# Optimization experiments

Measured on AMD Instinct MI355X. Metric: run time of the kernel, lower is better.

Reference implementation:

```python
import jax, jax.numpy as jnp
import numpy as np

M, K, N, R = 8192, 4096, 4096, 64  # tokens, in_features, out_features, pod_rank


def _unpack_int4(packed):
    """Unpack bytes (stored as int32 in [0,256)) into signed int4 values in [-8,7].
    Low nibble is element 2k, high nibble is element 2k+1."""
    b = packed.astype(jnp.int32)
    low = ((b & 0xF) ^ 8) - 8
    high = (((b >> 4) & 0xF) ^ 8) - 8
    out = jnp.stack([low, high], axis=-1)
    return out.reshape(packed.shape[:-1] + (packed.shape[-1] * 2,))


def setup_inputs() -> dict:
    key = jax.random.key(0)
    ks = jax.random.split(key, 7)
    x_quant = jax.random.randint(ks[0], (M, K // 2), 0, 256, dtype=jnp.int32)
    x_scale = jax.random.uniform(ks[1], (M,), dtype=jnp.float32) * 0.01 + 1e-4
    weight = jax.random.randint(ks[2], (N, K // 2), 0, 256, dtype=jnp.int32)
    weight_scales = jax.random.uniform(ks[3], (N, 1), dtype=jnp.float32) * 0.01 + 1e-4
    bias = jax.random.normal(ks[4], (N,), dtype=jnp.float32) * 0.02
    x_r = jax.random.normal(ks[5], (M, R), dtype=jnp.float32)
    w_outlier = jax.random.normal(ks[6], (N, R), dtype=jnp.float32) * 0.02
    return {"x_quant": x_quant, "x_scale": x_scale, "weight": weight,
            "weight_scales": weight_scales, "bias": bias, "x_r": x_r,
            "w_outlier": w_outlier}


def reference(x_quant, x_scale, weight, weight_scales, bias, x_r, w_outlier):
    xi = _unpack_int4(x_quant)          # [M, K] int32 in [-8,7]
    wi = _unpack_int4(weight)           # [N, K] int32 in [-8,7]
    y_int = jnp.matmul(xi, wi.T)        # [M, N] int32 accumulator
    # dequant: per-token activation scale * per-channel weight scale, plus bias
    y = (y_int.astype(jnp.float32) * x_scale[:, None] * weight_scales.reshape(1, -1)
         + bias[None, :])
    # fused low-rank outlier correction: addmm_(x_r, w_outlier.T)
    y = y + jnp.matmul(x_r, w_outlier.T)
    return y
```

## Files before the change

### kernel.cpp

```cpp
#include <hip/hip_runtime.h>
#include <hip/hip_fp16.h>

typedef int      v4i  __attribute__((ext_vector_type(4)));
typedef int      v2i  __attribute__((ext_vector_type(2)));
typedef int      v16i __attribute__((ext_vector_type(16)));
typedef float    v4f  __attribute__((ext_vector_type(4)));
typedef float    v16f __attribute__((ext_vector_type(16)));
typedef _Float16 v8h  __attribute__((ext_vector_type(8)));
typedef _Float16 v4h  __attribute__((ext_vector_type(4)));

#define MDIM 8192
#define NDIM 4096
#define KDIM 4096
#define RDIM 64
#define KW   (KDIM / 2)
#define NT   (KDIM / 128)

typedef const __attribute__((address_space(1))) char* gas_ptr;
typedef __attribute__((address_space(3))) char*       las_ptr;

__device__ __forceinline__ void unpack_w(v4i w, int& lo8, int& hi8) {
    unsigned p01 = __builtin_amdgcn_perm((unsigned)w.y, (unsigned)w.x, 0x0C0C0400u);
    unsigned p23 = __builtin_amdgcn_perm((unsigned)w.w, (unsigned)w.z, 0x0C0C0400u);
    unsigned b4  = __builtin_amdgcn_perm(p23, p01, 0x05040100u);
    unsigned lo = b4 & 0x0F0F0F0Fu;
    unsigned hi = (b4 >> 4) & 0x0F0F0F0Fu;
    lo8 = (int)(((lo ^ 0x08080808u) + 0x78787878u) ^ 0x80808080u);
    hi8 = (int)(((hi ^ 0x08080808u) + 0x78787878u) ^ 0x80808080u);
}

__global__ __launch_bounds__(256)
void repack_int4(const int* __restrict__ xq, const int* __restrict__ wq,
                 char* __restrict__ x8, char* __restrict__ w8)
{
    const size_t XCH = (size_t)MDIM * KW / 4;
    const size_t TCH = XCH + (size_t)NDIM * KW / 4;
    size_t stride = (size_t)gridDim.x * blockDim.x;
    for (size_t i = (size_t)blockIdx.x * blockDim.x + threadIdx.x; i < TCH; i += stride) {
        const int* src;
        char* dst;
        if (i < XCH) { src = xq + i * 4; dst = x8 + i * 8; }
        else { size_t j = i - XCH; src = wq + j * 4; dst = w8 + j * 8; }
        v4i w = *(const v4i*)src;
        int lo8, hi8;
        unpack_w(w, lo8, hi8);
        *(v2i*)dst = (v2i){lo8, hi8};
    }
}

__device__ __forceinline__ void stage2(const char* g, char* l, int kt, int ks) {
    const char* s = g + kt * 128 + ks * 64;
    __builtin_amdgcn_global_load_lds((gas_ptr)(const void*)s,
                                     (las_ptr)(void*)l, 16, 0, 0);
    __builtin_amdgcn_global_load_lds((gas_ptr)(const void*)(s + (size_t)128 * KDIM),
                                     (las_ptr)(void*)(l + 8192), 16, 0, 0);
}

#define BAR asm volatile("s_barrier" ::: "memory")
#define VM4 asm volatile("s_waitcnt vmcnt(4)" ::: "memory")
#define SGB(m, n) __builtin_amdgcn_sched_group_barrier(m, n, 0)

#define SGBSEQ do {                                                            \
    SGB(0x100, 2); SGB(0x8, 2); SGB(0x100, 2); SGB(0x8, 2);                    \
    SGB(0x100, 2); SGB(0x8, 2); SGB(0x100, 2); SGB(0x8, 2);                    \
    SGB(0x100, 2); SGB(0x8, 2); SGB(0x100, 2); SGB(0x8, 2);                    \
    SGB(0x30, 2);  SGB(0x8, 2); SGB(0x30, 2);  SGB(0x8, 2);                    \
} while (0)

#define READ_AB(DA, DB, PAR, KS_) do {                                         \
    const char* Ab_ = (const char*)Asub[PAR][KS_];                             \
    const char* Bb_ = (const char*)Bsub[PAR][KS_];                             \
    _Pragma("unroll")                                                          \
    for (int ii = 0; ii < 4; ++ii) {                                           \
        DA[ii][0] = *(const v4i*)(Ab_ + aoff + ii * 2048);                     \
        DA[ii][1] = *(const v4i*)(Ab_ + (aoff ^ 32) + ii * 2048);              \
    }                                                                          \
    _Pragma("unroll")                                                          \
    for (int jj = 0; jj < 2; ++jj) {                                           \
        DB[jj][0] = *(const v4i*)(Bb_ + boff + jj * 2048);                     \
        DB[jj][1] = *(const v4i*)(Bb_ + (boff ^ 32) + jj * 2048);              \
    }                                                                          \
} while (0)

#define MMA16(AS, BS)                                                          \
    _Pragma("unroll")                                                          \
    for (int ks_ = 0; ks_ < 2; ++ks_)                                          \
        _Pragma("unroll")                                                      \
        for (int ii = 0; ii < 4; ++ii)                                         \
            _Pragma("unroll")                                                  \
            for (int jj = 0; jj < 2; ++jj)                                     \
                acc[ii][jj] = __builtin_amdgcn_mfma_i32_32x32x32_i8(           \
                    AS[ii][ks_], BS[jj][ks_], acc[ii][jj], 0, 0, 0)

#define QPHASE(CA, CB, NA, NB, NPAR, NKS, SPAR, SKS, SKT) do {                 \
    READ_AB(NA, NB, NPAR, NKS);                                                \
    stage2(gA, &Asub[SPAR][SKS][ldsW], SKT, SKS);                              \
    stage2(gB, &Bsub[SPAR][SKS][ldsW], SKT, SKS);                              \
    MMA16(CA, CB);                                                             \
    SGBSEQ;                                                                    \
    VM4; BAR;                                                                  \
} while (0)

__global__ __launch_bounds__(512, 2)
void w4a4_g32(const char* __restrict__ x8, const char* __restrict__ w8,
              const float* __restrict__ xsc, const float* __restrict__ wsc,
              const float* __restrict__ bias, const float* __restrict__ xr,
              const float* __restrict__ wo, float* __restrict__ out)
{
    __shared__ __align__(16) char Asub[2][2][16384];
    __shared__ __align__(16) char Bsub[2][2][16384];
    __shared__ float xs_s[256];
    __shared__ float ws_s[256];
    __shared__ float bs_s[256];

    const int tid  = threadIdx.x;
    const int lane = tid & 63;
    const int wid  = tid >> 6;
    const int wm   = wid >> 2;
    const int wn   = wid & 3;

    const int s  = (blockIdx.x & 7) * 64 + (blockIdx.x >> 3);
    const int by = s >> 4;
    const int bxn = s & 15;

    if (tid < 256) {
        xs_s[tid] = xsc[by * 256 + tid];
    } else {
        int n = tid - 256;
        ws_s[n] = wsc[bxn * 256 + n];
        bs_s[n] = bias[bxn * 256 + n];
    }

    const int srow = wid * 16 + (lane >> 2);
    const int scol = ((lane & 3) * 16) ^ (((lane >> 3) & 3) << 4);
    const char* gA = x8 + (size_t)(by * 256 + srow) * KDIM + scol;
    const char* gB = w8 + (size_t)(bxn * 256 + srow) * KDIM + scol;
    const int ldsW = wid * 1024;

    const int l31 = lane & 31;
    const int kh  = lane >> 5;
    const int cks = (kh << 4) ^ (((l31 >> 1) & 3) << 4);
    const int aoff = (wm * 128 + l31) * 64 + cks;
    const int boff = (wn * 64  + l31) * 64 + cks;

    v16i acc[4][2];
#pragma unroll
    for (int i = 0; i < 4; ++i)
#pragma unroll
        for (int j = 0; j < 2; ++j)
#pragma unroll
            for (int r = 0; r < 16; ++r) acc[i][j][r] = 0;

    stage2(gA, &Asub[0][0][ldsW], 0, 0);
    stage2(gB, &Bsub[0][0][ldsW], 0, 0);
    stage2(gA, &Asub[0][1][ldsW], 0, 1);
    stage2(gB, &Bsub[0][1][ldsW], 0, 1);
    stage2(gA, &Asub[1][0][ldsW], 1, 0);
    stage2(gB, &Bsub[1][0][ldsW], 1, 0);
    VM4;
    BAR;

    v4i a0[4][2], b0[2][2], a1[4][2], b1[2][2];
    READ_AB(a0, b0, 0, 0);

    for (int it = 0; it < NT / 2; ++it) {
        const int kt1 = 2 * it + 1;
        const int kt2 = (2 * it + 2 < NT) ? 2 * it + 2 : NT - 1;
        const int kt3 = (2 * it + 3 < NT) ? 2 * it + 3 : NT - 1;
        QPHASE(a0, b0, a1, b1, 0, 1, 1, 1, kt1);
        QPHASE(a1, b1, a0, b0, 1, 0, 0, 0, kt2);
        QPHASE(a0, b0, a1, b1, 1, 1, 0, 1, kt2);
        QPHASE(a1, b1, a0, b0, 0, 0, 1, 0, kt3);
    }

    asm volatile("s_waitcnt vmcnt(0)" ::: "memory");
    BAR;

    char* Xh = (char*)&Asub[0][0][0];
    char* Wh = (char*)&Bsub[0][0][0];
    {
        const int rr = tid >> 3;
        const int cb = (tid & 7) * 16;
#pragma unroll
        for (int p = 0; p < 4; ++p) {
            const int row = p * 64 + rr;
            const int sw = cb ^ ((row & 7) << 4);
            v4f x0 = *(const v4f*)(xr + (size_t)(by * 256 + row) * RDIM + (cb >> 1));
            v4f x1 = *(const v4f*)(xr + (size_t)(by * 256 + row) * RDIM + (cb >> 1) + 4);
            v8h hx = {(_Float16)x0[0], (_Float16)x0[1], (_Float16)x0[2], (_Float16)x0[3],
                      (_Float16)x1[0], (_Float16)x1[1], (_Float16)x1[2], (_Float16)x1[3]};
            *(v8h*)(Xh + (size_t)row * 128 + sw) = hx;
            v4f w0 = *(const v4f*)(wo + (size_t)(bxn * 256 + row) * RDIM + (cb >> 1));
            v4f w1 = *(const v4f*)(wo + (size_t)(bxn * 256 + row) * RDIM + (cb >> 1) + 4);
            v8h hw = {(_Float16)w0[0], (_Float16)w0[1], (_Float16)w0[2], (_Float16)w0[3],
                      (_Float16)w1[0], (_Float16)w1[1], (_Float16)w1[2], (_Float16)w1[3]};
            *(v8h*)(Wh + (size_t)row * 128 + sw) = hw;
        }
    }

#pragma unroll
    for (int i = 0; i < 4; ++i) {
        const int r0 = wm * 128 + i * 32 + kh * 4;
#pragma unroll
        for (int j = 0; j < 2; ++j) {
            const int col = wn * 64 + j * 32 + l31;
            const float sw = ws_s[col];
            const float bz = bs_s[col];
            v16f f;
#pragma unroll
            for (int q = 0; q < 4; ++q) {
                const v4f xs4 = *(const v4f*)&xs_s[r0 + q * 8];
#pragma unroll
                for (int r = 0; r < 4; ++r)
                    f[q * 4 + r] = (float)acc[i][j][q * 4 + r] * xs4[r] * sw + bz;
            }
            acc[i][j] = __builtin_bit_cast(v16i, f);
        }
    }
    __syncthreads();

    const int obsw = (kh << 4) ^ ((l31 & 7) << 4);
#pragma unroll
    for (int ks = 0; ks < 4; ++ks) {
        v8h ah[4], bh[2];
#pragma unroll
        for (int i = 0; i < 4; ++i) {
            const int row = wm * 128 + i * 32 + l31;
            ah[i] = *(const v8h*)(Xh + (size_t)row * 128 + (obsw ^ (ks << 5)));
        }
#pragma unroll
        for (int j = 0; j < 2; ++j) {
            const int row = wn * 64 + j * 32 + l31;
            bh[j] = *(const v8h*)(Wh + (size_t)row * 128 + (obsw ^ (ks << 5)));
        }
#pragma unroll
        for (int i = 0; i < 4; ++i)
#pragma unroll
            for (int j = 0; j < 2; ++j) {
                v16f c = __builtin_bit_cast(v16f, acc[i][j]);
                c = __builtin_amdgcn_mfma_f32_32x32x16_f16(ah[i], bh[j], c, 0, 0, 0);
                acc[i][j] = __builtin_bit_cast(v16i, c);
            }
    }

    const int colb = bxn * 256 + wn * 64 + l31;
    const int rowb = by * 256 + wm * 128 + kh * 4;
#pragma unroll
    for (int i = 0; i < 4; ++i)
#pragma unroll
        for (int j = 0; j < 2; ++j) {
            v16f f = __builtin_bit_cast(v16f, acc[i][j]);
            const int col = colb + j * 32;
#pragma unroll
            for (int q = 0; q < 4; ++q) {
                const int row = rowb + i * 32 + q * 8;
#pragma unroll
                for (int r = 0; r < 4; ++r)
                    out[(size_t)(row + r) * NDIM + col] = f[q * 4 + r];
            }
        }
}

__global__ __launch_bounds__(256, 2)
void w4a4_fused(const int* __restrict__ xq, const float* __restrict__ xsc,
                const int* __restrict__ wq, const float* __restrict__ wsc,
                const float* __restrict__ bias, const float* __restrict__ xr,
                const float* __restrict__ wo, float* __restrict__ out)
{
    __shared__ __align__(16) char As[128 * 144];
    __shared__ __align__(16) char Bs[128 * 144];
    __shared__ float xs_s[128];
    __shared__ float ws_s[128];
    __shared__ float bs_s[128];

    const int tid  = threadIdx.x;
    const int lane = tid & 63;
    const int wid  = tid >> 6;
    const int wm   = wid >> 1;
    const int wn   = wid & 1;
    const int bx   = blockIdx.x % (NDIM / 128);
    const int by   = blockIdx.x / (NDIM / 128);

    const int srow   = tid >> 4;
    const int schunk = tid & 15;

    if (tid < 128) {
        xs_s[tid] = xsc[by * 128 + tid];
    } else {
        int n = tid - 128;
        ws_s[n] = wsc[bx * 128 + n];
        bs_s[n] = bias[bx * 128 + n];
    }

    const int* gA = xq + (size_t)(by * 128 + srow) * KW + schunk * 4;
    const int* gB = wq + (size_t)(bx * 128 + srow) * KW + schunk * 4;
    char* lA = As + srow * 144 + schunk * 8;
    char* lB = Bs + srow * 144 + schunk * 8;

    v4i acc[4][4];
#pragma unroll
    for (int i = 0; i < 4; ++i)
#pragma unroll
        for (int j = 0; j < 4; ++j) acc[i][j] = (v4i){0, 0, 0, 0};

    const int lr = lane & 15;
    const int lkb = (lane >> 4) * 16;

    for (int kt = 0; kt < KDIM / 128; ++kt) {
#pragma unroll
        for (int p = 0; p < 8; ++p) {
            v4i w = *(const v4i*)(gA + (size_t)p * 16 * KW + kt * 64);
            int lo8, hi8;
            unpack_w(w, lo8, hi8);
            *(v2i*)(lA + p * 16 * 144) = (v2i){lo8, hi8};
        }
#pragma unroll
        for (int p = 0; p < 8; ++p) {
            v4i w = *(const v4i*)(gB + (size_t)p * 16 * KW + kt * 64);
            int lo8, hi8;
            unpack_w(w, lo8, hi8);
            *(v2i*)(lB + p * 16 * 144) = (v2i){lo8, hi8};
        }
        __syncthreads();
#pragma unroll
        for (int ks = 0; ks < 2; ++ks) {
            v4i av[4], bv[4];
#pragma unroll
            for (int i = 0; i < 4; ++i)
                av[i] = *(const v4i*)(As + (wm * 64 + i * 16 + lr) * 144 + ks * 64 + lkb);
#pragma unroll
            for (int j = 0; j < 4; ++j)
                bv[j] = *(const v4i*)(Bs + (wn * 64 + j * 16 + lr) * 144 + ks * 64 + lkb);
#pragma unroll
            for (int i = 0; i < 4; ++i)
#pragma unroll
                for (int j = 0; j < 4; ++j)
                    acc[i][j] = __builtin_amdgcn_mfma_i32_16x16x64_i8(av[i], bv[j], acc[i][j], 0, 0, 0);
        }
        __syncthreads();
    }

    _Float16* Xh = (_Float16*)As;
    _Float16* Wh = (_Float16*)Bs;
#pragma unroll
    for (int p = 0; p < 8; ++p) {
        int row = p * 16 + srow;
        float4 vx = *(const float4*)(xr + (size_t)(by * 128 + row) * RDIM + schunk * 4);
        *(v4h*)(Xh + row * 72 + schunk * 4) =
            (v4h){(_Float16)vx.x, (_Float16)vx.y, (_Float16)vx.z, (_Float16)vx.w};
        float4 vw = *(const float4*)(wo + (size_t)(bx * 128 + row) * RDIM + schunk * 4);
        *(v4h*)(Wh + row * 72 + schunk * 4) =
            (v4h){(_Float16)vw.x, (_Float16)vw.y, (_Float16)vw.z, (_Float16)vw.w};
    }
    __syncthreads();

    v4f facc[4][4];
#pragma unroll
    for (int i = 0; i < 4; ++i)
#pragma unroll
        for (int j = 0; j < 4; ++j) facc[i][j] = (v4f){0.f, 0.f, 0.f, 0.f};

    const int lkh = (lane >> 4) * 8;
#pragma unroll
    for (int ks = 0; ks < 2; ++ks) {
        v8h ah[4], bh[4];
#pragma unroll
        for (int i = 0; i < 4; ++i)
            ah[i] = *(const v8h*)(Xh + (wm * 64 + i * 16 + lr) * 72 + ks * 32 + lkh);
#pragma unroll
        for (int j = 0; j < 4; ++j)
            bh[j] = *(const v8h*)(Wh + (wn * 64 + j * 16 + lr) * 72 + ks * 32 + lkh);
#pragma unroll
        for (int i = 0; i < 4; ++i)
#pragma unroll
            for (int j = 0; j < 4; ++j)
                facc[i][j] = __builtin_amdgcn_mfma_f32_16x16x32_f16(ah[i], bh[j], facc[i][j], 0, 0, 0);
    }

#pragma unroll
    for (int i = 0; i < 4; ++i) {
        int row0 = wm * 64 + i * 16 + (lane >> 4) * 4;
#pragma unroll
        for (int j = 0; j < 4; ++j) {
            int col = wn * 64 + j * 16 + lr;
            float sw = ws_s[col];
            float bz = bs_s[col];
#pragma unroll
            for (int r = 0; r < 4; ++r) {
                int row = row0 + r;
                float v = (float)acc[i][j][r] * xs_s[row] * sw + bz + facc[i][j][r];
                out[(size_t)(by * 128 + row) * NDIM + (bx * 128 + col)] = v;
            }
        }
    }
}

extern "C" void kernel_launch(void* const* d_in, const int* in_sizes, int n_in,
                              void* d_out, int out_size, void* d_ws, size_t ws_size,
                              hipStream_t stream) {
    const int*   xq   = (const int*)d_in[0];
    const float* xsc  = (const float*)d_in[1];
    const int*   wq   = (const int*)d_in[2];
    const float* wsc  = (const float*)d_in[3];
    const float* bias = (const float*)d_in[4];
    const float* xr   = (const float*)d_in[5];
    const float* wo   = (const float*)d_in[6];
    float* out = (float*)d_out;

    const size_t X8 = (size_t)MDIM * KDIM;
    const size_t W8 = (size_t)NDIM * KDIM;

    if (ws_size >= X8 + W8) {
        char* x8 = (char*)d_ws;
        char* w8 = x8 + X8;
        repack_int4<<<2048, 256, 0, stream>>>(xq, wq, x8, w8);
        w4a4_g32<<<(MDIM / 256) * (NDIM / 256), 512, 0, stream>>>(
            x8, w8, xsc, wsc, bias, xr, wo, out);
    } else {
        w4a4_fused<<<(MDIM / 128) * (NDIM / 128), 256, 0, stream>>>(
            xq, xsc, wq, wsc, bias, xr, wo, out);
    }
}
```

Before: 177.2 us.

## Restructure int8 GEMM mainloop with full-K-tile LDS buffers and staggered A/B prefetch

Replaces the four quarter-phase pipeline (two 64-byte K halves per buffer, vmcnt(4) waits) with full 128-byte K-tile LDS buffers, using a new 128-byte-row XOR swizzle and 4-row-strided global_load_lds staging. Each half-iteration stages only B or only A for a future tile, reads the next fragment half from LDS, and interleaves those reads with MFMAs. It then waits with lgkmcnt(0)/vmcnt(0) and a barrier. The aim is fewer barriers per K tile and a better LDS read/MFMA interleave, at the cost of full vmcnt(0) drains that may expose global load latency.

Result: no change. 175.4 us (-1.1%).

```diff
diff --git a/kernel.cpp b/kernel.cpp
--- a/kernel.cpp
+++ b/kernel.cpp
@@ -48,67 +48,62 @@
     }
 }
 
-__device__ __forceinline__ void stage2(const char* g, char* l, int kt, int ks) {
-    const char* s = g + kt * 128 + ks * 64;
-    __builtin_amdgcn_global_load_lds((gas_ptr)(const void*)s,
-                                     (las_ptr)(void*)l, 16, 0, 0);
-    __builtin_amdgcn_global_load_lds((gas_ptr)(const void*)(s + (size_t)128 * KDIM),
-                                     (las_ptr)(void*)(l + 8192), 16, 0, 0);
-}
-
-#define BAR asm volatile("s_barrier" ::: "memory")
-#define VM4 asm volatile("s_waitcnt vmcnt(4)" ::: "memory")
+__device__ __forceinline__ void stage4(const char* g, char* l, int kt) {
+#pragma unroll
+    for (int q = 0; q < 4; ++q)
+        __builtin_amdgcn_global_load_lds(
+            (gas_ptr)(const void*)(g + (size_t)(q * 8) * KDIM + kt * 128),
+            (las_ptr)(void*)(l + q * 1024), 16, 0, 0);
+}
+
+#define BAR   asm volatile("s_barrier" ::: "memory")
+#define VM0   asm volatile("s_waitcnt vmcnt(0)" ::: "memory")
+#define LGKM0 do { asm volatile("s_waitcnt lgkmcnt(0)" ::: "memory");          \
+                   __builtin_amdgcn_sched_barrier(0); } while (0)
 #define SGB(m, n) __builtin_amdgcn_sched_group_barrier(m, n, 0)
 
 #define SGBSEQ do {                                                            \
-    SGB(0x100, 2); SGB(0x8, 2); SGB(0x100, 2); SGB(0x8, 2);                    \
-    SGB(0x100, 2); SGB(0x8, 2); SGB(0x100, 2); SGB(0x8, 2);                    \
-    SGB(0x100, 2); SGB(0x8, 2); SGB(0x100, 2); SGB(0x8, 2);                    \
-    SGB(0x30, 2);  SGB(0x8, 2); SGB(0x30, 2);  SGB(0x8, 2);                    \
+    SGB(0x30, 1); SGB(0x8, 1); SGB(0x30, 1); SGB(0x8, 1);                      \
+    SGB(0x30, 1); SGB(0x8, 1); SGB(0x30, 1); SGB(0x8, 1);                      \
+    SGB(0x100, 3); SGB(0x8, 3); SGB(0x100, 3); SGB(0x8, 3);                    \
+    SGB(0x100, 3); SGB(0x8, 3); SGB(0x100, 3); SGB(0x8, 3);                    \
 } while (0)
 
-#define READ_AB(DA, DB, PAR, KS_) do {                                         \
-    const char* Ab_ = (const char*)Asub[PAR][KS_];                             \
-    const char* Bb_ = (const char*)Bsub[PAR][KS_];                             \
+#define READF(FA, FB, PAR, H) do {                                             \
+    const char* Ab_ = (const char*)Abuf[PAR];                                  \
+    const char* Bb_ = (const char*)Bbuf[PAR];                                  \
     _Pragma("unroll")                                                          \
-    for (int ii = 0; ii < 4; ++ii) {                                           \
-        DA[ii][0] = *(const v4i*)(Ab_ + aoff + ii * 2048);                     \
-        DA[ii][1] = *(const v4i*)(Ab_ + (aoff ^ 32) + ii * 2048);              \
-    }                                                                          \
+    for (int m_ = 0; m_ < 4; ++m_)                                             \
+        _Pragma("unroll")                                                      \
+        for (int ks_ = 0; ks_ < 2; ++ks_)                                      \
+            FA[m_ * 2 + ks_] = *(const v4i*)(Ab_ + aoffM + m_ * 4096 +         \
+                                   (((H) * 64 + ks_ * 32) ^ cef));             \
     _Pragma("unroll")                                                          \
-    for (int jj = 0; jj < 2; ++jj) {                                           \
-        DB[jj][0] = *(const v4i*)(Bb_ + boff + jj * 2048);                     \
-        DB[jj][1] = *(const v4i*)(Bb_ + (boff ^ 32) + jj * 2048);              \
-    }                                                                          \
+    for (int j_ = 0; j_ < 2; ++j_)                                             \
+        _Pragma("unroll")                                                      \
+        for (int ks_ = 0; ks_ < 2; ++ks_)                                      \
+            FB[j_ * 2 + ks_] = *(const v4i*)(Bb_ + boffN + j_ * 4096 +         \
+                                   (((H) * 64 + ks_ * 32) ^ cef));             \
 } while (0)
 
-#define MMA16(AS, BS)                                                          \
+#define MMA16(FA, FB)                                                          \
     _Pragma("unroll")                                                          \
     for (int ks_ = 0; ks_ < 2; ++ks_)                                          \
         _Pragma("unroll")                                                      \
-        for (int ii = 0; ii < 4; ++ii)                                         \
+        for (int m_ = 0; m_ < 4; ++m_)                                         \
             _Pragma("unroll")                                                  \
-            for (int jj = 0; jj < 2; ++jj)                                     \
-                acc[ii][jj] = __builtin_amdgcn_mfma_i32_32x32x32_i8(           \
-                    AS[ii][ks_], BS[jj][ks_], acc[ii][jj], 0, 0, 0)
-
-#define QPHASE(CA, CB, NA, NB, NPAR, NKS, SPAR, SKS, SKT) do {                 \
-    READ_AB(NA, NB, NPAR, NKS);                                                \
-    stage2(gA, &Asub[SPAR][SKS][ldsW], SKT, SKS);                              \
-    stage2(gB, &Bsub[SPAR][SKS][ldsW], SKT, SKS);                              \
-    MMA16(CA, CB);                                                             \
-    SGBSEQ;                                                                    \
-    VM4; BAR;                                                                  \
-} while (0)
+            for (int j_ = 0; j_ < 2; ++j_)                                     \
+                acc[m_][j_] = __builtin_amdgcn_mfma_i32_32x32x32_i8(           \
+                    FA[m_ * 2 + ks_], FB[j_ * 2 + ks_], acc[m_][j_], 0, 0, 0)
 
 __global__ __launch_bounds__(512, 2)
-void w4a4_g32(const char* __restrict__ x8, const char* __restrict__ w8,
-              const float* __restrict__ xsc, const float* __restrict__ wsc,
-              const float* __restrict__ bias, const float* __restrict__ xr,
-              const float* __restrict__ wo, float* __restrict__ out)
+void w4a4_g32b(const char* __restrict__ x8, const char* __restrict__ w8,
+               const float* __restrict__ xsc, const float* __restrict__ wsc,
+               const float* __restrict__ bias, const float* __restrict__ xr,
+               const float* __restrict__ wo, float* __restrict__ out)
 {
-    __shared__ __align__(16) char Asub[2][2][16384];
-    __shared__ __align__(16) char Bsub[2][2][16384];
+    __shared__ __align__(16) char Abuf[2][32768];
+    __shared__ __align__(16) char Bbuf[2][32768];
     __shared__ float xs_s[256];
     __shared__ float ws_s[256];
     __shared__ float bs_s[256];
@@ -131,17 +126,16 @@
         bs_s[n] = bias[bxn * 256 + n];
     }
 
-    const int srow = wid * 16 + (lane >> 2);
-    const int scol = ((lane & 3) * 16) ^ (((lane >> 3) & 3) << 4);
-    const char* gA = x8 + (size_t)(by * 256 + srow) * KDIM + scol;
-    const char* gB = w8 + (size_t)(bxn * 256 + srow) * KDIM + scol;
-    const int ldsW = wid * 1024;
+    const int scol = ((lane & 7) << 4) ^ (((lane >> 3) & 7) << 4);
+    const char* gA = x8 + (size_t)(by * 256 + wid * 32 + (lane >> 3)) * KDIM + scol;
+    const char* gB = w8 + (size_t)(bxn * 256 + wid * 32 + (lane >> 3)) * KDIM + scol;
+    const int ldsW = wid * 4096;
 
     const int l31 = lane & 31;
     const int kh  = lane >> 5;
-    const int cks = (kh << 4) ^ (((l31 >> 1) & 3) << 4);
-    const int aoff = (wm * 128 + l31) * 64 + cks;
-    const int boff = (wn * 64  + l31) * 64 + cks;
+    const int cef  = (kh << 4) ^ ((l31 & 7) << 4);
+    const int aoffM = wm * 16384 + l31 * 128;
+    const int boffN = wn * 8192  + l31 * 128;
 
     v16i acc[4][2];
 #pragma unroll
@@ -151,33 +145,33 @@
 #pragma unroll
             for (int r = 0; r < 16; ++r) acc[i][j][r] = 0;
 
-    stage2(gA, &Asub[0][0][ldsW], 0, 0);
-    stage2(gB, &Bsub[0][0][ldsW], 0, 0);
-    stage2(gA, &Asub[0][1][ldsW], 0, 1);
-    stage2(gB, &Bsub[0][1][ldsW], 0, 1);
-    stage2(gA, &Asub[1][0][ldsW], 1, 0);
-    stage2(gB, &Bsub[1][0][ldsW], 1, 0);
-    VM4;
+    stage4(gA, &Abuf[0][ldsW], 0);
+    stage4(gB, &Bbuf[0][ldsW], 0);
+    stage4(gA, &Abuf[1][ldsW], 1);
+    VM0; BAR;
+
+    v4i f0A[8], f0B[4], f1A[8], f1B[4];
+    READF(f0A, f0B, 0, 0);
+    LGKM0;
     BAR;
 
-    v4i a0[4][2], b0[2][2], a1[4][2], b1[2][2];
-    READ_AB(a0, b0, 0, 0);
-
-    for (int it = 0; it < NT / 2; ++it) {
-        const int kt1 = 2 * it + 1;
-        const int kt2 = (2 * it + 2 < NT) ? 2 * it + 2 : NT - 1;
-        const int kt3 = (2 * it + 3 < NT) ? 2 * it + 3 : NT - 1;
-        QPHASE(a0, b0, a1, b1, 0, 1, 1, 1, kt1);
-        QPHASE(a1, b1, a0, b0, 1, 0, 0, 0, kt2);
-        QPHASE(a0, b0, a1, b1, 1, 1, 0, 1, kt2);
-        QPHASE(a1, b1, a0, b0, 0, 0, 1, 0, kt3);
-    }
-
-    asm volatile("s_waitcnt vmcnt(0)" ::: "memory");
-    BAR;
-
-    char* Xh = (char*)&Asub[0][0][0];
-    char* Wh = (char*)&Bsub[0][0][0];
+    for (int P = 0; P < NT; ++P) {
+        const int ktB = (P + 1 < NT) ? P + 1 : NT - 1;
+        const int ktA = (P + 2 < NT) ? P + 2 : NT - 1;
+        stage4(gB, &Bbuf[(P + 1) & 1][ldsW], ktB);
+        READF(f1A, f1B, P & 1, 1);
+        MMA16(f0A, f0B);
+        SGBSEQ;
+        LGKM0; VM0; BAR;
+        stage4(gA, &Abuf[P & 1][ldsW], ktA);
+        READF(f0A, f0B, (P + 1) & 1, 0);
+        MMA16(f1A, f1B);
+        SGBSEQ;
+        LGKM0; VM0; BAR;
+    }
+
+    char* Xh = (char*)&Abuf[0][0];
+    char* Wh = (char*)&Bbuf[0][0];
     {
         const int rr = tid >> 3;
         const int cb = (tid & 7) * 16;
@@ -414,7 +408,7 @@
         char* x8 = (char*)d_ws;
         char* w8 = x8 + X8;
         repack_int4<<<2048, 256, 0, stream>>>(xq, wq, x8, w8);
-        w4a4_g32<<<(MDIM / 256) * (NDIM / 256), 512, 0, stream>>>(
+        w4a4_g32b<<<(MDIM / 256) * (NDIM / 256), 512, 0, stream>>>(
             x8, w8, xsc, wsc, bias, xr, wo, out);
     } else {
         w4a4_fused<<<(MDIM / 128) * (NDIM / 128), 256, 0, stream>>>(
```
